# Kernel tuning notes

Measured on AMD Instinct MI355X. Metric: run time of the kernel, lower is better.

Reference implementation:

```python
import jax, jax.numpy as jnp
import numpy as np

V, E, H, K = 8000, 100, 64, 17  # vocab, embed, hidden, num_tags (fixed by source)
B, T = 256, 512


def setup_inputs() -> dict:
    key = jax.random.key(0)
    ks = jax.random.split(key, 16)
    g = lambda i, shape: (jax.random.normal(ks[i], shape, jnp.float32) * 0.1)
    data = jax.random.randint(ks[0], (B, T), 0, V).astype(jnp.int32)
    mask = jnp.ones((B, T), dtype=bool)
    return {
        "data": data,
        "mask": mask,
        "emb": g(1, (V, E)),
        # PyTorch LSTM layout: gates stacked [i, f, g, o] along dim 0
        "Wih_f": g(2, (4 * H, E)), "Whh_f": g(3, (4 * H, H)),
        "bih_f": g(4, (4 * H,)), "bhh_f": g(5, (4 * H,)),
        "Wih_b": g(6, (4 * H, E)), "Whh_b": g(7, (4 * H, H)),
        "bih_b": g(8, (4 * H,)), "bhh_b": g(9, (4 * H,)),
        "W_out": g(10, (K, 2 * H)), "b_out": g(11, (K,)),
        "trans": g(12, (K, K)),            # trans[i, j] = score of i -> j
        "start_trans": g(13, (K,)),
        "end_trans": g(14, (K,)),
    }


def _lstm_dir(x, Wih, Whh, bih, bhh, reverse):
    # x: [B, T, E] -> hidden states [B, T, H]
    Bx, Tx, _ = x.shape
    Hx = Whh.shape[1]
    xs = jnp.swapaxes(x, 0, 1)  # [T, B, E]

    def step(carry, xt):
        h, c = carry
        gates = xt @ Wih.T + h @ Whh.T + bih + bhh  # [B, 4H]
        i, f, g, o = jnp.split(gates, 4, axis=-1)
        c = jax.nn.sigmoid(f) * c + jax.nn.sigmoid(i) * jnp.tanh(g)
        h = jax.nn.sigmoid(o) * jnp.tanh(c)
        return (h, c), h

    init = (jnp.zeros((Bx, Hx), x.dtype), jnp.zeros((Bx, Hx), x.dtype))
    _, hs = jax.lax.scan(step, init, xs, reverse=reverse)
    return jnp.swapaxes(hs, 0, 1)  # [B, T, H]


def _emissions(data, emb, Wih_f, Whh_f, bih_f, bhh_f, Wih_b, Whh_b, bih_b, bhh_b, W_out, b_out):
    x = emb[data]                                         # [B, T, E]
    hf = _lstm_dir(x, Wih_f, Whh_f, bih_f, bhh_f, False)  # [B, T, H]
    hb = _lstm_dir(x, Wih_b, Whh_b, bih_b, bhh_b, True)   # [B, T, H]
    h = jnp.concatenate([hf, hb], axis=-1)                # [B, T, 2H]
    return h @ W_out.T + b_out                            # [B, T, K]


def _viterbi(emission, mask, trans, start_trans, end_trans):
    Bx, Tx, Kx = emission.shape
    score = start_trans[None, :] + emission[:, 0]         # [B, K]
    em = jnp.swapaxes(emission, 0, 1)[1:]                 # [T-1, B, K]
    mk = jnp.swapaxes(mask, 0, 1)[1:]                     # [T-1, B]
    ident = jnp.arange(Kx)

    def step(score, inp):
        emit_t, m_t = inp
        # cand[b, i, j] = score[b, i] + trans[i, j] + emit_t[b, j]
        cand = score[:, :, None] + trans[None] + emit_t[:, None, :]
        new = cand.max(axis=1)
        bp = cand.argmax(axis=1)
        score = jnp.where(m_t[:, None], new, score)
        bp = jnp.where(m_t[:, None], bp, ident[None, :])
        return score, bp

    score, bps = jax.lax.scan(step, score, (em, mk))       # bps: [T-1, B, K]
    final = score + end_trans[None, :]
    best_score = final.max(axis=1)                         # [B]
    last = final.argmax(axis=1)                            # [B]

    def back(tag, bp_t):
        prev = jnp.take_along_axis(bp_t, tag[:, None], axis=1)[:, 0]
        return prev, prev

    _, prevs = jax.lax.scan(back, last, bps, reverse=True)  # [T-1, B]
    paths = jnp.concatenate([prevs, last[None, :]], axis=0).T  # [B, T]
    return best_score, paths


def reference(data, mask, emb, Wih_f, Whh_f, bih_f, bhh_f, Wih_b, Whh_b, bih_b, bhh_b,
              W_out, b_out, trans, start_trans, end_trans):
    emission = _emissions(data, emb, Wih_f, Whh_f, bih_f, bhh_f,
                          Wih_b, Whh_b, bih_b, bhh_b, W_out, b_out)
    return _viterbi(emission, mask, trans, start_trans, end_trans)
```

## Files before the change

kernel.cpp:

```cpp
#include <hip/hip_runtime.h>
#include <hip/hip_bf16.h>

typedef unsigned int u32;
typedef unsigned char u8;

#define B_ 256
#define T_ 512
#define E_ 100
#define H_ 64
#define K_ 17
#define V_ 8000

#define WS_G     0
#define WS_H     16384000
#define WS_EMIT  83492864
#define WS_BP    92405760
#define WS_LAST  96600064

#define PINF4(v) asm volatile("" : "+v"((v).x), "+v"((v).y), "+v"((v).z), "+v"((v).w))

__device__ __forceinline__ float qp_xor1(float v) {
  int r = __builtin_amdgcn_update_dpp(0, __builtin_bit_cast(int, v), 0xB1, 0xF, 0xF, true);
  return __builtin_bit_cast(float, r);
}
__device__ __forceinline__ float qp_xor2(float v) {
  int r = __builtin_amdgcn_update_dpp(0, __builtin_bit_cast(int, v), 0x4E, 0xF, 0xF, true);
  return __builtin_bit_cast(float, r);
}

__global__ __launch_bounds__(256)
__attribute__((amdgpu_waves_per_eu(2, 2)))
void k1_build_G(
    const float* __restrict__ emb,
    const float* __restrict__ Wih_f,
    const float* __restrict__ bih_f,
    const float* __restrict__ bhh_f,
    const float* __restrict__ Wih_b,
    const float* __restrict__ bih_b,
    const float* __restrict__ bhh_b,
    float* __restrict__ G)
{
  __shared__ float xl[32 * E_];
  int v0 = blockIdx.x * 32;
  int dir = blockIdx.y;
  int tid = threadIdx.x;
  const float* Wih = dir ? Wih_b : Wih_f;
  const float* bih = dir ? bih_b : bih_f;
  const float* bhh = dir ? bhh_b : bhh_f;

  for (int i = tid; i < 32 * E_; i += 256) xl[i] = emb[v0 * E_ + i];

  int u = tid >> 2, g = tid & 3;
  int row = (g << 6) + u;
  const float* wr = Wih + row * E_;
#define LDA(name, q) float4 name = *reinterpret_cast<const float4*>(wr + 4 * (q)); PINF4(name)
  LDA(A0,0);  LDA(A1,1);  LDA(A2,2);  LDA(A3,3);  LDA(A4,4);
  LDA(A5,5);  LDA(A6,6);  LDA(A7,7);  LDA(A8,8);  LDA(A9,9);
  LDA(A10,10);LDA(A11,11);LDA(A12,12);LDA(A13,13);LDA(A14,14);
  LDA(A15,15);LDA(A16,16);LDA(A17,17);LDA(A18,18);LDA(A19,19);
  LDA(A20,20);LDA(A21,21);LDA(A22,22);LDA(A23,23);LDA(A24,24);
#undef LDA
  float bias = __fadd_rn(bih[row], bhh[row]);
  __syncthreads();

  float* Gd = G + (size_t)dir * V_ * 256;
  for (int vi = 0; vi < 32; ++vi) {
    const float* xp = &xl[vi * E_];
    float a0 = bias, a1 = 0.f, a2 = 0.f, a3 = 0.f;
#define K1F(Aq, q) { float4 x4 = *reinterpret_cast<const float4*>(xp + 4 * (q)); \
    a0 = fmaf(Aq.x, x4.x, a0); a1 = fmaf(Aq.y, x4.y, a1); \
    a2 = fmaf(Aq.z, x4.z, a2); a3 = fmaf(Aq.w, x4.w, a3); }
    K1F(A0,0)  K1F(A1,1)  K1F(A2,2)  K1F(A3,3)  K1F(A4,4)
    K1F(A5,5)  K1F(A6,6)  K1F(A7,7)  K1F(A8,8)  K1F(A9,9)
    K1F(A10,10)K1F(A11,11)K1F(A12,12)K1F(A13,13)K1F(A14,14)
    K1F(A15,15)K1F(A16,16)K1F(A17,17)K1F(A18,18)K1F(A19,19)
    K1F(A20,20)K1F(A21,21)K1F(A22,22)K1F(A23,23)K1F(A24,24)
#undef K1F
    Gd[(v0 + vi) * 256 + tid] = (a0 + a1) + (a2 + a3);
  }
}

__global__ __launch_bounds__(256)
__attribute__((amdgpu_waves_per_eu(2, 2)))
void k2_lstm(
    const int* __restrict__ data,
    const float* __restrict__ G,
    const float* __restrict__ Whh_f,
    const float* __restrict__ Whh_b,
    float* __restrict__ hout)
{
  __shared__ __align__(16) float hls[2][64];
  __shared__ int tok_lds[T_ + 8];
  int bid = blockIdx.x;
  int b = bid & 255;
  int dir = bid >> 8;
  int tid = threadIdx.x;
  int w = tid >> 6, l = tid & 63;
  int ul = l >> 2;
  int kq = l & 3;
  int u = (w << 4) + ul;
  const float* Whh = dir ? Whh_b : Whh_f;
  const float* wb = Whh + u * 64 + (kq << 4);

#define LDW(name, g, q) float4 name = *reinterpret_cast<const float4*>(wb + (g) * 4096 + 4 * (q)); PINF4(name)
  LDW(W00,0,0); LDW(W01,0,1); LDW(W02,0,2); LDW(W03,0,3);
  LDW(W10,1,0); LDW(W11,1,1); LDW(W12,1,2); LDW(W13,1,3);
  LDW(W20,2,0); LDW(W21,2,1); LDW(W22,2,2); LDW(W23,2,3);
  LDW(W30,3,0); LDW(W31,3,1); LDW(W32,3,2); LDW(W33,3,3);
#undef LDW

  const int* tokp = data + b * T_;
  for (int i = tid; i < T_; i += 256)
    tok_lds[i] = tokp[dir ? (T_ - 1 - i) : i];
  if (tid < 8) tok_lds[T_ + tid] = 0;
  if (tid < 64) hls[0][tid] = 0.0f;
  __syncthreads();

  float c = 0.0f;
  const float* Gd = G + (size_t)dir * V_ * 256;
  float* hob = hout + ((size_t)(dir * B_ + b)) * T_ * H_;
  float* hop = hob + (dir ? (T_ - 1) * H_ : 0) + u;
  int hstep = dir ? -H_ : H_;
  const float L2E = 1.4426950408889634f;

  float4 gq0, gq1, gq2, gq3;
  {
    int t0 = __builtin_amdgcn_readfirstlane(tok_lds[0]);
    int t1 = __builtin_amdgcn_readfirstlane(tok_lds[1]);
    int t2 = __builtin_amdgcn_readfirstlane(tok_lds[2]);
    int t3 = __builtin_amdgcn_readfirstlane(tok_lds[3]);
    gq0 = *reinterpret_cast<const float4*>(Gd + ((size_t)t0 << 8) + (u << 2));
    gq1 = *reinterpret_cast<const float4*>(Gd + ((size_t)t1 << 8) + (u << 2));
    gq2 = *reinterpret_cast<const float4*>(Gd + ((size_t)t2 << 8) + (u << 2));
    gq3 = *reinterpret_cast<const float4*>(Gd + ((size_t)t3 << 8) + (u << 2));
  }
  int tk_next = tok_lds[4];

  int cur = 0;
  for (int s = 0; s < T_; ++s) {
    int tokn = __builtin_amdgcn_readfirstlane(tk_next);
    float4 gq4 = *reinterpret_cast<const float4*>(Gd + ((size_t)tokn << 8) + (u << 2));
    tk_next = tok_lds[s + 5];

    const float* hq = hls[cur] + (kq << 4);
    float4 h0 = *reinterpret_cast<const float4*>(hq + 0);
    float4 h1 = *reinterpret_cast<const float4*>(hq + 4);
    float4 h2 = *reinterpret_cast<const float4*>(hq + 8);
    float4 h3 = *reinterpret_cast<const float4*>(hq + 12);
#define GDOT(res, Wa, Wb, Wc, Wd) float res; { \
    float b0 = Wa.x * h0.x; float b1 = Wa.y * h0.y; float b2 = Wa.z * h0.z; float b3 = Wa.w * h0.w; \
    b0 = fmaf(Wb.x, h1.x, b0); b1 = fmaf(Wb.y, h1.y, b1); b2 = fmaf(Wb.z, h1.z, b2); b3 = fmaf(Wb.w, h1.w, b3); \
    b0 = fmaf(Wc.x, h2.x, b0); b1 = fmaf(Wc.y, h2.y, b1); b2 = fmaf(Wc.z, h2.z, b2); b3 = fmaf(Wc.w, h2.w, b3); \
    b0 = fmaf(Wd.x, h3.x, b0); b1 = fmaf(Wd.y, h3.y, b1); b2 = fmaf(Wd.z, h3.z, b2); b3 = fmaf(Wd.w, h3.w, b3); \
    res = (b0 + b1) + (b2 + b3); }
    GDOT(acc0, W00, W01, W02, W03)
    GDOT(acc1, W10, W11, W12, W13)
    GDOT(acc2, W20, W21, W22, W23)
    GDOT(acc3, W30, W31, W32, W33)
#undef GDOT
    float t0 = acc0 + qp_xor1(acc0); float f0 = t0 + qp_xor2(t0);
    float t1 = acc1 + qp_xor1(acc1); float f1 = t1 + qp_xor2(t1);
    float t2 = acc2 + qp_xor1(acc2); float f2 = t2 + qp_xor2(t2);
    float t3 = acc3 + qp_xor1(acc3); float f3 = t3 + qp_xor2(t3);
    float xi = f0 + gq0.x;
    float xf = f1 + gq0.y;
    float xg = f2 + gq0.z;
    float xo = f3 + gq0.w;
    float si = __builtin_amdgcn_rcpf(1.0f + __builtin_amdgcn_exp2f(xi * (-L2E)));
    float sf = __builtin_amdgcn_rcpf(1.0f + __builtin_amdgcn_exp2f(xf * (-L2E)));
    float tg = fmaf(2.0f, __builtin_amdgcn_rcpf(1.0f + __builtin_amdgcn_exp2f(xg * (-2.0f * L2E))), -1.0f);
    float so = __builtin_amdgcn_rcpf(1.0f + __builtin_amdgcn_exp2f(xo * (-L2E)));
    c = __fadd_rn(__fmul_rn(sf, c), __fmul_rn(si, tg));
    float tc = fmaf(2.0f, __builtin_amdgcn_rcpf(1.0f + __builtin_amdgcn_exp2f(c * (-2.0f * L2E))), -1.0f);
    float hn = __fmul_rn(so, tc);
    if (kq == 0) {
      hls[cur ^ 1][u] = hn;
      *hop = hn;
    }
    hop += hstep;
    asm volatile("s_waitcnt lgkmcnt(0)\n\ts_barrier" ::: "memory");
    cur ^= 1;
    gq0 = gq1; gq1 = gq2; gq2 = gq3; gq3 = gq4;
  }
}

__global__ __launch_bounds__(256) void k3_emit(
    const float* __restrict__ hbuf,
    const float* __restrict__ W_out,
    const float* __restrict__ b_out,
    float* __restrict__ emit)
{
  __shared__ float hl[64][132];
  __shared__ float Wl[17][132];
  int tid = threadIdx.x;
  int p0 = blockIdx.x * 64;
  const float* hf = hbuf;
  const float* hb = hbuf + (size_t)B_ * T_ * H_;
#pragma unroll
  for (int i = 0; i < 4; ++i) {
    int idx = tid + i * 256;
    int pos = idx >> 4, e4 = idx & 15;
    float4 v = reinterpret_cast<const float4*>(hf + (size_t)p0 * 64)[idx];
    *reinterpret_cast<float4*>(&hl[pos][e4 * 4]) = v;
    float4 v2 = reinterpret_cast<const float4*>(hb + (size_t)p0 * 64)[idx];
    *reinterpret_cast<float4*>(&hl[pos][64 + e4 * 4]) = v2;
  }
  for (int i = tid; i < 17 * 128; i += 256) {
    int k = i >> 7, e = i & 127;
    Wl[k][e] = W_out[i];
  }
  __syncthreads();

  int pos = tid >> 2, ks = tid & 3;
  float acc[5] = {0.f, 0.f, 0.f, 0.f, 0.f};
#pragma unroll
  for (int e4 = 0; e4 < 32; ++e4) {
    float4 x4 = *reinterpret_cast<const float4*>(&hl[pos][e4 * 4]);
#pragma unroll
    for (int kk = 0; kk < 5; ++kk) {
      int k = ks + kk * 4;
      if (k < K_) {
        float4 w4 = *reinterpret_cast<const float4*>(&Wl[k][e4 * 4]);
        acc[kk] = fmaf(x4.x, w4.x, acc[kk]);
        acc[kk] = fmaf(x4.y, w4.y, acc[kk]);
        acc[kk] = fmaf(x4.z, w4.z, acc[kk]);
        acc[kk] = fmaf(x4.w, w4.w, acc[kk]);
      }
    }
  }
#pragma unroll
  for (int kk = 0; kk < 5; ++kk) {
    int k = ks + kk * 4;
    if (k < K_)
      emit[(size_t)(p0 + pos) * K_ + k] = __fadd_rn(acc[kk], b_out[k]);
  }
}

#define AMAX(vA, iA, vB, iB) { bool tk_ = (vB) > (vA); if (tk_) { vA = (vB); iA = (iB); } }

__global__ __launch_bounds__(64) void k4_viterbi(
    const float* __restrict__ emit,
    const float* __restrict__ trans,
    const float* __restrict__ start_trans,
    const float* __restrict__ end_trans,
    u8* __restrict__ bp,
    int* __restrict__ last,
    float* __restrict__ out)
{
  int b = blockIdx.x;
  int l = threadIdx.x;
  int ic = l >> 5;
  int hbase = l & 32;
  int j = l & 31;
  int jc = (j < K_) ? j : 0;
  int i0 = ic ? 9 : 0;
  int cnt = ic ? 8 : 9;
  float tr0 = trans[(i0 + 0) * K_ + jc];
  float tr1 = trans[(i0 + 1) * K_ + jc];
  float tr2 = trans[(i0 + 2) * K_ + jc];
  float tr3 = trans[(i0 + 3) * K_ + jc];
  float tr4 = trans[(i0 + 4) * K_ + jc];
  float tr5 = trans[(i0 + 5) * K_ + jc];
  float tr6 = trans[(i0 + 6) * K_ + jc];
  float tr7 = trans[(i0 + 7) * K_ + jc];
  float tr8 = (cnt > 8) ? trans[(i0 + 8) * K_ + jc] : -__builtin_inff();
  asm volatile("" : "+v"(tr0), "+v"(tr1), "+v"(tr2), "+v"(tr3), "+v"(tr4),
                    "+v"(tr5), "+v"(tr6), "+v"(tr7), "+v"(tr8));
  const float* eb = emit + (size_t)b * T_ * K_;
  float endt = end_trans[jc];
  float s = __fadd_rn(start_trans[jc], eb[jc]);
  u8* bpb = bp + (size_t)b * T_ * 32;
  float er0 = eb[1 * K_ + jc];
  float er1 = eb[2 * K_ + jc];
  float er2 = eb[3 * K_ + jc];
  float er3 = eb[4 * K_ + jc];

  for (int t = 1; t < T_; ++t) {
    float ej = er0;
    er0 = er1; er1 = er2; er2 = er3;
    if (t + 4 < T_) er3 = eb[(size_t)(t + 4) * K_ + jc];
    float p0 = __shfl(s, hbase + i0 + 0, 64);
    float p1 = __shfl(s, hbase + i0 + 1, 64);
    float p2 = __shfl(s, hbase + i0 + 2, 64);
    float p3 = __shfl(s, hbase + i0 + 3, 64);
    float p4 = __shfl(s, hbase + i0 + 4, 64);
    float p5 = __shfl(s, hbase + i0 + 5, 64);
    float p6 = __shfl(s, hbase + i0 + 6, 64);
    float p7 = __shfl(s, hbase + i0 + 7, 64);
    float p8 = __shfl(s, hbase + i0 + 8, 64);
    float c0 = __fadd_rn(__fadd_rn(p0, tr0), ej);
    float c1 = __fadd_rn(__fadd_rn(p1, tr1), ej);
    float c2 = __fadd_rn(__fadd_rn(p2, tr2), ej);
    float c3 = __fadd_rn(__fadd_rn(p3, tr3), ej);
    float c4 = __fadd_rn(__fadd_rn(p4, tr4), ej);
    float c5 = __fadd_rn(__fadd_rn(p5, tr5), ej);
    float c6 = __fadd_rn(__fadd_rn(p6, tr6), ej);
    float c7 = __fadd_rn(__fadd_rn(p7, tr7), ej);
    float c8 = __fadd_rn(__fadd_rn(p8, tr8), ej);
    float v01 = c0; int x01 = i0;     AMAX(v01, x01, c1, i0 + 1);
    float v23 = c2; int x23 = i0 + 2; AMAX(v23, x23, c3, i0 + 3);
    float v45 = c4; int x45 = i0 + 4; AMAX(v45, x45, c5, i0 + 5);
    float v67 = c6; int x67 = i0 + 6; AMAX(v67, x67, c7, i0 + 7);
    AMAX(v01, x01, v23, x23);
    AMAX(v45, x45, v67, x67);
    AMAX(v01, x01, v45, x45);
    AMAX(v01, x01, c8, i0 + 8);
    float m = v01; int idx = x01;
    float m2 = __shfl_xor(m, 32, 64);
    int idx2 = __shfl_xor(idx, 32, 64);
    bool take = (m2 > m) || ((m2 == m) && (idx2 < idx));
    if (take) { m = m2; idx = idx2; }
    s = m;
    if (ic == 0 && j < K_) bpb[(size_t)(t - 1) * 32 + j] = (u8)idx;
  }
  float fin = __fadd_rn(s, endt);
  float bm = __shfl(fin, hbase, 64);
  int bi = 0;
#pragma unroll
  for (int jj = 1; jj < K_; ++jj) {
    float v = __shfl(fin, hbase + jj, 64);
    if (v > bm) { bm = v; bi = jj; }
  }
  if (l == 0) {
    out[b] = bm;
    last[b] = bi;
    out[256 + (size_t)b * T_ + (T_ - 1)] = (float)bi;
  }
}

__global__ __launch_bounds__(64) void k5_backtrace(
    const u8* __restrict__ bp,
    const int* __restrict__ last,
    float* __restrict__ out)
{
  int b = blockIdx.x * 64 + threadIdx.x;
  const u8* base = bp + (size_t)b * T_ * 32;
  int tag = last[b];
  float* ob = out + 256 + (size_t)b * T_;
  uint4 A0[8], A1[8];
  u32 B0[8], B1[8];
#pragma unroll
  for (int q = 0; q < 8; ++q) {
    const u8* p = base + (size_t)(510 - q) * 32;
    A0[q] = *reinterpret_cast<const uint4*>(p);
    B0[q] = *reinterpret_cast<const u32*>(p + 16);
  }
  int t0 = 510;
  for (int pair = 0; pair < 32; ++pair) {
#pragma unroll
    for (int q = 0; q < 8; ++q) {
      int tn = t0 - 8 - q;
      if (tn >= 0) {
        const u8* p = base + (size_t)tn * 32;
        A1[q] = *reinterpret_cast<const uint4*>(p);
        B1[q] = *reinterpret_cast<const u32*>(p + 16);
      }
    }
#pragma unroll
    for (int q = 0; q < 8; ++q) {
      int t = t0 - q;
      if (t >= 0) {
        uint4 Av = A0[q]; u32 Bw = B0[q];
        u32 dw = (tag < 8) ? ((tag < 4) ? Av.x : Av.y) : ((tag < 12) ? Av.z : Av.w);
        dw = (tag < 16) ? dw : Bw;
        tag = (int)((dw >> ((tag & 3) * 8)) & 0xffu);
        ob[t] = (float)tag;
      }
    }
#pragma unroll
    for (int q = 0; q < 8; ++q) {
      int tn = t0 - 16 - q;
      if (tn >= 0) {
        const u8* p = base + (size_t)tn * 32;
        A0[q] = *reinterpret_cast<const uint4*>(p);
        B0[q] = *reinterpret_cast<const u32*>(p + 16);
      }
    }
#pragma unroll
    for (int q = 0; q < 8; ++q) {
      int t = t0 - 8 - q;
      if (t >= 0) {
        uint4 Av = A1[q]; u32 Bw = B1[q];
        u32 dw = (tag < 8) ? ((tag < 4) ? Av.x : Av.y) : ((tag < 12) ? Av.z : Av.w);
        dw = (tag < 16) ? dw : Bw;
        tag = (int)((dw >> ((tag & 3) * 8)) & 0xffu);
        ob[t] = (float)tag;
      }
    }
    t0 -= 16;
  }
}

extern "C" void kernel_launch(void* const* d_in, const int* in_sizes, int n_in,
                              void* d_out, int out_size, void* d_ws, size_t ws_size,
                              hipStream_t stream) {
  const int*   data  = (const int*)d_in[0];
  const float* emb   = (const float*)d_in[2];
  const float* Wih_f = (const float*)d_in[3];
  const float* Whh_f = (const float*)d_in[4];
  const float* bih_f = (const float*)d_in[5];
  const float* bhh_f = (const float*)d_in[6];
  const float* Wih_b = (const float*)d_in[7];
  const float* Whh_b = (const float*)d_in[8];
  const float* bih_b = (const float*)d_in[9];
  const float* bhh_b = (const float*)d_in[10];
  const float* W_out = (const float*)d_in[11];
  const float* b_out = (const float*)d_in[12];
  const float* trans = (const float*)d_in[13];
  const float* start_trans = (const float*)d_in[14];
  const float* end_trans   = (const float*)d_in[15];

  char* ws = (char*)d_ws;
  float* G    = (float*)(ws + WS_G);
  float* hbuf = (float*)(ws + WS_H);
  float* emit = (float*)(ws + WS_EMIT);
  u8*    bp   = (u8*)(ws + WS_BP);
  int*   lastp = (int*)(ws + WS_LAST);
  float* out = (float*)d_out;

  k1_build_G<<<dim3(250, 2), 256, 0, stream>>>(emb, Wih_f, bih_f, bhh_f,
                                               Wih_b, bih_b, bhh_b, G);
  k2_lstm<<<512, 256, 0, stream>>>(data, G, Whh_f, Whh_b, hbuf);
  k3_emit<<<2048, 256, 0, stream>>>(hbuf, W_out, b_out, emit);
  k4_viterbi<<<256, 64, 0, stream>>>(emit, trans, start_trans, end_trans,
                                     bp, lastp, out);
  k5_backtrace<<<4, 64, 0, stream>>>(bp, lastp, out);
}
```

Before: 668.2 us.

## Use packed FMA in LSTM, register-resident emit projection, readlane-based Viterbi

```diff
diff --git a/kernel.cpp b/kernel.cpp
--- a/kernel.cpp
+++ b/kernel.cpp
@@ -3,6 +3,7 @@
 
 typedef unsigned int u32;
 typedef unsigned char u8;
+typedef __attribute__((ext_vector_type(2))) float f2;
 
 #define B_ 256
 #define T_ 512
@@ -18,6 +19,8 @@
 #define WS_LAST  96600064
 
 #define PINF4(v) asm volatile("" : "+v"((v).x), "+v"((v).y), "+v"((v).z), "+v"((v).w))
+#define PINF2(v) asm volatile("" : "+v"(v))
+#define FMA2(a, b, c) __builtin_elementwise_fma((a), (b), (c))
 
 __device__ __forceinline__ float qp_xor1(float v) {
   int r = __builtin_amdgcn_update_dpp(0, __builtin_bit_cast(int, v), 0xB1, 0xF, 0xF, true);
@@ -26,6 +29,9 @@
 __device__ __forceinline__ float qp_xor2(float v) {
   int r = __builtin_amdgcn_update_dpp(0, __builtin_bit_cast(int, v), 0x4E, 0xF, 0xF, true);
   return __builtin_bit_cast(float, r);
+}
+__device__ __forceinline__ float rdl(float v, int lane) {
+  return __builtin_bit_cast(float, __builtin_amdgcn_readlane(__builtin_bit_cast(int, v), lane));
 }
 
 __global__ __launch_bounds__(256)
@@ -100,13 +106,16 @@
   int kq = l & 3;
   int u = (w << 4) + ul;
   const float* Whh = dir ? Whh_b : Whh_f;
-  const float* wb = Whh + u * 64 + (kq << 4);
-
-#define LDW(name, g, q) float4 name = *reinterpret_cast<const float4*>(wb + (g) * 4096 + 4 * (q)); PINF4(name)
-  LDW(W00,0,0); LDW(W01,0,1); LDW(W02,0,2); LDW(W03,0,3);
-  LDW(W10,1,0); LDW(W11,1,1); LDW(W12,1,2); LDW(W13,1,3);
-  LDW(W20,2,0); LDW(W21,2,1); LDW(W22,2,2); LDW(W23,2,3);
-  LDW(W30,3,0); LDW(W31,3,1); LDW(W32,3,2); LDW(W33,3,3);
+  const f2* wb2 = reinterpret_cast<const f2*>(Whh + u * 64 + (kq << 4));
+
+#define LDW(pre, g) \
+  f2 pre##0 = wb2[(g)*2048+0]; f2 pre##1 = wb2[(g)*2048+1]; \
+  f2 pre##2 = wb2[(g)*2048+2]; f2 pre##3 = wb2[(g)*2048+3]; \
+  f2 pre##4 = wb2[(g)*2048+4]; f2 pre##5 = wb2[(g)*2048+5]; \
+  f2 pre##6 = wb2[(g)*2048+6]; f2 pre##7 = wb2[(g)*2048+7]; \
+  PINF2(pre##0); PINF2(pre##1); PINF2(pre##2); PINF2(pre##3); \
+  PINF2(pre##4); PINF2(pre##5); PINF2(pre##6); PINF2(pre##7)
+  LDW(Wa, 0); LDW(Wb, 1); LDW(Wc, 2); LDW(Wd, 3);
 #undef LDW
 
   const int* tokp = data + b * T_;
@@ -137,34 +146,31 @@
   int tk_next = tok_lds[4];
 
   int cur = 0;
+#pragma unroll 2
   for (int s = 0; s < T_; ++s) {
     int tokn = __builtin_amdgcn_readfirstlane(tk_next);
     float4 gq4 = *reinterpret_cast<const float4*>(Gd + ((size_t)tokn << 8) + (u << 2));
     tk_next = tok_lds[s + 5];
 
-    const float* hq = hls[cur] + (kq << 4);
-    float4 h0 = *reinterpret_cast<const float4*>(hq + 0);
-    float4 h1 = *reinterpret_cast<const float4*>(hq + 4);
-    float4 h2 = *reinterpret_cast<const float4*>(hq + 8);
-    float4 h3 = *reinterpret_cast<const float4*>(hq + 12);
-#define GDOT(res, Wa, Wb, Wc, Wd) float res; { \
-    float b0 = Wa.x * h0.x; float b1 = Wa.y * h0.y; float b2 = Wa.z * h0.z; float b3 = Wa.w * h0.w; \
-    b0 = fmaf(Wb.x, h1.x, b0); b1 = fmaf(Wb.y, h1.y, b1); b2 = fmaf(Wb.z, h1.z, b2); b3 = fmaf(Wb.w, h1.w, b3); \
-    b0 = fmaf(Wc.x, h2.x, b0); b1 = fmaf(Wc.y, h2.y, b1); b2 = fmaf(Wc.z, h2.z, b2); b3 = fmaf(Wc.w, h2.w, b3); \
-    b0 = fmaf(Wd.x, h3.x, b0); b1 = fmaf(Wd.y, h3.y, b1); b2 = fmaf(Wd.z, h3.z, b2); b3 = fmaf(Wd.w, h3.w, b3); \
-    res = (b0 + b1) + (b2 + b3); }
-    GDOT(acc0, W00, W01, W02, W03)
-    GDOT(acc1, W10, W11, W12, W13)
-    GDOT(acc2, W20, W21, W22, W23)
-    GDOT(acc3, W30, W31, W32, W33)
+    const f2* hq2 = reinterpret_cast<const f2*>(hls[cur] + (kq << 4));
+    f2 ha = hq2[0], hb2 = hq2[1], hc = hq2[2], hd = hq2[3];
+    f2 he = hq2[4], hf2 = hq2[5], hg = hq2[6], hh = hq2[7];
+#define GDOT(res, W0,W1,W2,W3,W4,W5,W6,W7) float res; { \
+    f2 c01 = W0 * ha;  c01 = FMA2(W2, hc, c01); c01 = FMA2(W4, he, c01); c01 = FMA2(W6, hg, c01); \
+    f2 c23 = W1 * hb2; c23 = FMA2(W3, hd, c23); c23 = FMA2(W5, hf2, c23); c23 = FMA2(W7, hh, c23); \
+    res = (c01.x + c01.y) + (c23.x + c23.y); }
+    GDOT(acc0, Wa0,Wa1,Wa2,Wa3,Wa4,Wa5,Wa6,Wa7)
+    GDOT(acc1, Wb0,Wb1,Wb2,Wb3,Wb4,Wb5,Wb6,Wb7)
+    GDOT(acc2, Wc0,Wc1,Wc2,Wc3,Wc4,Wc5,Wc6,Wc7)
+    GDOT(acc3, Wd0,Wd1,Wd2,Wd3,Wd4,Wd5,Wd6,Wd7)
 #undef GDOT
     float t0 = acc0 + qp_xor1(acc0); float f0 = t0 + qp_xor2(t0);
     float t1 = acc1 + qp_xor1(acc1); float f1 = t1 + qp_xor2(t1);
-    float t2 = acc2 + qp_xor1(acc2); float f2 = t2 + qp_xor2(t2);
+    float t2 = acc2 + qp_xor1(acc2); float f2v = t2 + qp_xor2(t2);
     float t3 = acc3 + qp_xor1(acc3); float f3 = t3 + qp_xor2(t3);
     float xi = f0 + gq0.x;
     float xf = f1 + gq0.y;
-    float xg = f2 + gq0.z;
+    float xg = f2v + gq0.z;
     float xo = f3 + gq0.w;
     float si = __builtin_amdgcn_rcpf(1.0f + __builtin_amdgcn_exp2f(xi * (-L2E)));
     float sf = __builtin_amdgcn_rcpf(1.0f + __builtin_amdgcn_exp2f(xf * (-L2E)));
@@ -184,55 +190,45 @@
   }
 }
 
-__global__ __launch_bounds__(256) void k3_emit(
+__global__ __launch_bounds__(256)
+__attribute__((amdgpu_waves_per_eu(2, 2)))
+void k3_emit(
     const float* __restrict__ hbuf,
     const float* __restrict__ W_out,
     const float* __restrict__ b_out,
     float* __restrict__ emit)
 {
-  __shared__ float hl[64][132];
-  __shared__ float Wl[17][132];
-  int tid = threadIdx.x;
-  int p0 = blockIdx.x * 64;
-  const float* hf = hbuf;
-  const float* hb = hbuf + (size_t)B_ * T_ * H_;
-#pragma unroll
-  for (int i = 0; i < 4; ++i) {
-    int idx = tid + i * 256;
-    int pos = idx >> 4, e4 = idx & 15;
-    float4 v = reinterpret_cast<const float4*>(hf + (size_t)p0 * 64)[idx];
-    *reinterpret_cast<float4*>(&hl[pos][e4 * 4]) = v;
-    float4 v2 = reinterpret_cast<const float4*>(hb + (size_t)p0 * 64)[idx];
-    *reinterpret_cast<float4*>(&hl[pos][64 + e4 * 4]) = v2;
-  }
-  for (int i = tid; i < 17 * 128; i += 256) {
-    int k = i >> 7, e = i & 127;
-    Wl[k][e] = W_out[i];
-  }
-  __syncthreads();
-
-  int pos = tid >> 2, ks = tid & 3;
-  float acc[5] = {0.f, 0.f, 0.f, 0.f, 0.f};
-#pragma unroll
-  for (int e4 = 0; e4 < 32; ++e4) {
-    float4 x4 = *reinterpret_cast<const float4*>(&hl[pos][e4 * 4]);
-#pragma unroll
-    for (int kk = 0; kk < 5; ++kk) {
-      int k = ks + kk * 4;
-      if (k < K_) {
-        float4 w4 = *reinterpret_cast<const float4*>(&Wl[k][e4 * 4]);
-        acc[kk] = fmaf(x4.x, w4.x, acc[kk]);
-        acc[kk] = fmaf(x4.y, w4.y, acc[kk]);
-        acc[kk] = fmaf(x4.z, w4.z, acc[kk]);
-        acc[kk] = fmaf(x4.w, w4.w, acc[kk]);
-      }
-    }
-  }
-#pragma unroll
-  for (int kk = 0; kk < 5; ++kk) {
-    int k = ks + kk * 4;
-    if (k < K_)
-      emit[(size_t)(p0 + pos) * K_ + k] = __fadd_rn(acc[kk], b_out[k]);
+  int pos = blockIdx.x * 256 + threadIdx.x;
+  const float* hfp = hbuf + (size_t)pos * 64;
+  const float* hbp = hbuf + (size_t)B_ * T_ * 64 + (size_t)pos * 64;
+#define LDH(name, base, q) float4 name = *reinterpret_cast<const float4*>((base) + 4 * (q)); PINF4(name)
+  LDH(H0, hfp,0);  LDH(H1, hfp,1);  LDH(H2, hfp,2);  LDH(H3, hfp,3);
+  LDH(H4, hfp,4);  LDH(H5, hfp,5);  LDH(H6, hfp,6);  LDH(H7, hfp,7);
+  LDH(H8, hfp,8);  LDH(H9, hfp,9);  LDH(H10,hfp,10); LDH(H11,hfp,11);
+  LDH(H12,hfp,12); LDH(H13,hfp,13); LDH(H14,hfp,14); LDH(H15,hfp,15);
+  LDH(H16,hbp,0);  LDH(H17,hbp,1);  LDH(H18,hbp,2);  LDH(H19,hbp,3);
+  LDH(H20,hbp,4);  LDH(H21,hbp,5);  LDH(H22,hbp,6);  LDH(H23,hbp,7);
+  LDH(H24,hbp,8);  LDH(H25,hbp,9);  LDH(H26,hbp,10); LDH(H27,hbp,11);
+  LDH(H28,hbp,12); LDH(H29,hbp,13); LDH(H30,hbp,14); LDH(H31,hbp,15);
+#undef LDH
+  float* ep = emit + (size_t)pos * K_;
+#pragma unroll 1
+  for (int k = 0; k < K_; ++k) {
+    const float* wk = W_out + k * 128;
+    float a0 = 0.f, a1 = 0.f, a2 = 0.f, a3 = 0.f;
+#define K3F(Hq, q) { \
+    a0 = fmaf(Hq.x, wk[4*(q)+0], a0); a1 = fmaf(Hq.y, wk[4*(q)+1], a1); \
+    a2 = fmaf(Hq.z, wk[4*(q)+2], a2); a3 = fmaf(Hq.w, wk[4*(q)+3], a3); }
+    K3F(H0,0)  K3F(H1,1)  K3F(H2,2)  K3F(H3,3)
+    K3F(H4,4)  K3F(H5,5)  K3F(H6,6)  K3F(H7,7)
+    K3F(H8,8)  K3F(H9,9)  K3F(H10,10)K3F(H11,11)
+    K3F(H12,12)K3F(H13,13)K3F(H14,14)K3F(H15,15)
+    K3F(H16,16)K3F(H17,17)K3F(H18,18)K3F(H19,19)
+    K3F(H20,20)K3F(H21,21)K3F(H22,22)K3F(H23,23)
+    K3F(H24,24)K3F(H25,25)K3F(H26,26)K3F(H27,27)
+    K3F(H28,28)K3F(H29,29)K3F(H30,30)K3F(H31,31)
+#undef K3F
+    ep[k] = __fadd_rn((a0 + a1) + (a2 + a3), b_out[k]);
   }
 }
 
@@ -249,82 +245,95 @@
 {
   int b = blockIdx.x;
   int l = threadIdx.x;
-  int ic = l >> 5;
-  int hbase = l & 32;
-  int j = l & 31;
-  int jc = (j < K_) ? j : 0;
-  int i0 = ic ? 9 : 0;
-  int cnt = ic ? 8 : 9;
-  float tr0 = trans[(i0 + 0) * K_ + jc];
-  float tr1 = trans[(i0 + 1) * K_ + jc];
-  float tr2 = trans[(i0 + 2) * K_ + jc];
-  float tr3 = trans[(i0 + 3) * K_ + jc];
-  float tr4 = trans[(i0 + 4) * K_ + jc];
-  float tr5 = trans[(i0 + 5) * K_ + jc];
-  float tr6 = trans[(i0 + 6) * K_ + jc];
-  float tr7 = trans[(i0 + 7) * K_ + jc];
-  float tr8 = (cnt > 8) ? trans[(i0 + 8) * K_ + jc] : -__builtin_inff();
-  asm volatile("" : "+v"(tr0), "+v"(tr1), "+v"(tr2), "+v"(tr3), "+v"(tr4),
-                    "+v"(tr5), "+v"(tr6), "+v"(tr7), "+v"(tr8));
+  int jc = (l < K_) ? l : 0;
+  float tr0  = trans[ 0 * K_ + jc], tr1  = trans[ 1 * K_ + jc];
+  float tr2  = trans[ 2 * K_ + jc], tr3  = trans[ 3 * K_ + jc];
+  float tr4  = trans[ 4 * K_ + jc], tr5  = trans[ 5 * K_ + jc];
+  float tr6  = trans[ 6 * K_ + jc], tr7  = trans[ 7 * K_ + jc];
+  float tr8  = trans[ 8 * K_ + jc], tr9  = trans[ 9 * K_ + jc];
+  float tr10 = trans[10 * K_ + jc], tr11 = trans[11 * K_ + jc];
+  float tr12 = trans[12 * K_ + jc], tr13 = trans[13 * K_ + jc];
+  float tr14 = trans[14 * K_ + jc], tr15 = trans[15 * K_ + jc];
+  float tr16 = trans[16 * K_ + jc];
   const float* eb = emit + (size_t)b * T_ * K_;
   float endt = end_trans[jc];
   float s = __fadd_rn(start_trans[jc], eb[jc]);
   u8* bpb = bp + (size_t)b * T_ * 32;
-  float er0 = eb[1 * K_ + jc];
-  float er1 = eb[2 * K_ + jc];
-  float er2 = eb[3 * K_ + jc];
-  float er3 = eb[4 * K_ + jc];
-
+  float er0 = eb[1 * K_ + jc], er1 = eb[2 * K_ + jc];
+  float er2 = eb[3 * K_ + jc], er3 = eb[4 * K_ + jc];
+  float er4 = eb[5 * K_ + jc], er5 = eb[6 * K_ + jc];
+  float er6 = eb[7 * K_ + jc], er7 = eb[8 * K_ + jc];
+
+#pragma unroll 4
   for (int t = 1; t < T_; ++t) {
     float ej = er0;
-    er0 = er1; er1 = er2; er2 = er3;
-    if (t + 4 < T_) er3 = eb[(size_t)(t + 4) * K_ + jc];
-    float p0 = __shfl(s, hbase + i0 + 0, 64);
-    float p1 = __shfl(s, hbase + i0 + 1, 64);
-    float p2 = __shfl(s, hbase + i0 + 2, 64);
-    float p3 = __shfl(s, hbase + i0 + 3, 64);
-    float p4 = __shfl(s, hbase + i0 + 4, 64);
-    float p5 = __shfl(s, hbase + i0 + 5, 64);
-    float p6 = __shfl(s, hbase + i0 + 6, 64);
-    float p7 = __shfl(s, hbase + i0 + 7, 64);
-    float p8 = __shfl(s, hbase + i0 + 8, 64);
-    float c0 = __fadd_rn(__fadd_rn(p0, tr0), ej);
-    float c1 = __fadd_rn(__fadd_rn(p1, tr1), ej);
-    float c2 = __fadd_rn(__fadd_rn(p2, tr2), ej);
-    float c3 = __fadd_rn(__fadd_rn(p3, tr3), ej);
-    float c4 = __fadd_rn(__fadd_rn(p4, tr4), ej);
-    float c5 = __fadd_rn(__fadd_rn(p5, tr5), ej);
-    float c6 = __fadd_rn(__fadd_rn(p6, tr6), ej);
-    float c7 = __fadd_rn(__fadd_rn(p7, tr7), ej);
-    float c8 = __fadd_rn(__fadd_rn(p8, tr8), ej);
-    float v01 = c0; int x01 = i0;     AMAX(v01, x01, c1, i0 + 1);
-    float v23 = c2; int x23 = i0 + 2; AMAX(v23, x23, c3, i0 + 3);
-    float v45 = c4; int x45 = i0 + 4; AMAX(v45, x45, c5, i0 + 5);
-    float v67 = c6; int x67 = i0 + 6; AMAX(v67, x67, c7, i0 + 7);
-    AMAX(v01, x01, v23, x23);
-    AMAX(v45, x45, v67, x67);
-    AMAX(v01, x01, v45, x45);
-    AMAX(v01, x01, c8, i0 + 8);
-    float m = v01; int idx = x01;
-    float m2 = __shfl_xor(m, 32, 64);
-    int idx2 = __shfl_xor(idx, 32, 64);
-    bool take = (m2 > m) || ((m2 == m) && (idx2 < idx));
-    if (take) { m = m2; idx = idx2; }
-    s = m;
-    if (ic == 0 && j < K_) bpb[(size_t)(t - 1) * 32 + j] = (u8)idx;
+    er0 = er1; er1 = er2; er2 = er3; er3 = er4;
+    er4 = er5; er5 = er6; er6 = er7;
+    int tn = (t + 8 < T_) ? (t + 8) : (T_ - 1);
+    er7 = eb[(size_t)tn * K_ + jc];
+    float sg0  = rdl(s, 0),  sg1  = rdl(s, 1),  sg2  = rdl(s, 2);
+    float sg3  = rdl(s, 3),  sg4  = rdl(s, 4),  sg5  = rdl(s, 5);
+    float sg6  = rdl(s, 6),  sg7  = rdl(s, 7),  sg8  = rdl(s, 8);
+    float sg9  = rdl(s, 9),  sg10 = rdl(s, 10), sg11 = rdl(s, 11);
+    float sg12 = rdl(s, 12), sg13 = rdl(s, 13), sg14 = rdl(s, 14);
+    float sg15 = rdl(s, 15), sg16 = rdl(s, 16);
+    float c0  = __fadd_rn(__fadd_rn(sg0,  tr0),  ej);
+    float c1  = __fadd_rn(__fadd_rn(sg1,  tr1),  ej);
+    float c2  = __fadd_rn(__fadd_rn(sg2,  tr2),  ej);
+    float c3  = __fadd_rn(__fadd_rn(sg3,  tr3),  ej);
+    float c4  = __fadd_rn(__fadd_rn(sg4,  tr4),  ej);
+    float c5  = __fadd_rn(__fadd_rn(sg5,  tr5),  ej);
+    float c6  = __fadd_rn(__fadd_rn(sg6,  tr6),  ej);
+    float c7  = __fadd_rn(__fadd_rn(sg7,  tr7),  ej);
+    float c8  = __fadd_rn(__fadd_rn(sg8,  tr8),  ej);
+    float c9  = __fadd_rn(__fadd_rn(sg9,  tr9),  ej);
+    float c10 = __fadd_rn(__fadd_rn(sg10, tr10), ej);
+    float c11 = __fadd_rn(__fadd_rn(sg11, tr11), ej);
+    float c12 = __fadd_rn(__fadd_rn(sg12, tr12), ej);
+    float c13 = __fadd_rn(__fadd_rn(sg13, tr13), ej);
+    float c14 = __fadd_rn(__fadd_rn(sg14, tr14), ej);
+    float c15 = __fadd_rn(__fadd_rn(sg15, tr15), ej);
+    float c16 = __fadd_rn(__fadd_rn(sg16, tr16), ej);
+    float v0 = c0;  int x0 = 0;  AMAX(v0, x0, c1, 1);
+    float v1 = c2;  int x1 = 2;  AMAX(v1, x1, c3, 3);
+    float v2 = c4;  int x2 = 4;  AMAX(v2, x2, c5, 5);
+    float v3 = c6;  int x3 = 6;  AMAX(v3, x3, c7, 7);
+    float v4 = c8;  int x4 = 8;  AMAX(v4, x4, c9, 9);
+    float v5 = c10; int x5 = 10; AMAX(v5, x5, c11, 11);
+    float v6 = c12; int x6 = 12; AMAX(v6, x6, c13, 13);
+    float v7 = c14; int x7 = 14; AMAX(v7, x7, c15, 15);
+    AMAX(v0, x0, v1, x1); AMAX(v2, x2, v3, x3);
+    AMAX(v4, x4, v5, x5); AMAX(v6, x6, v7, x7);
+    AMAX(v0, x0, v2, x2); AMAX(v4, x4, v6, x6);
+    AMAX(v0, x0, v4, x4);
+    AMAX(v0, x0, c16, 16);
+    s = v0;
+    if (l < K_) bpb[(size_t)(t - 1) * 32 + l] = (u8)x0;
   }
   float fin = __fadd_rn(s, endt);
-  float bm = __shfl(fin, hbase, 64);
-  int bi = 0;
-#pragma unroll
-  for (int jj = 1; jj < K_; ++jj) {
-    float v = __shfl(fin, hbase + jj, 64);
-    if (v > bm) { bm = v; bi = jj; }
-  }
+  float g0  = rdl(fin, 0),  g1  = rdl(fin, 1),  g2  = rdl(fin, 2);
+  float g3  = rdl(fin, 3),  g4  = rdl(fin, 4),  g5  = rdl(fin, 5);
+  float g6  = rdl(fin, 6),  g7  = rdl(fin, 7),  g8  = rdl(fin, 8);
+  float g9  = rdl(fin, 9),  g10 = rdl(fin, 10), g11 = rdl(fin, 11);
+  float g12 = rdl(fin, 12), g13 = rdl(fin, 13), g14 = rdl(fin, 14);
+  float g15 = rdl(fin, 15), g16 = rdl(fin, 16);
+  float w0 = g0;  int y0 = 0;  AMAX(w0, y0, g1, 1);
+  float w1 = g2;  int y1 = 2;  AMAX(w1, y1, g3, 3);
+  float w2 = g4;  int y2 = 4;  AMAX(w2, y2, g5, 5);
+  float w3 = g6;  int y3 = 6;  AMAX(w3, y3, g7, 7);
+  float w4 = g8;  int y4 = 8;  AMAX(w4, y4, g9, 9);
+  float w5 = g10; int y5 = 10; AMAX(w5, y5, g11, 11);
+  float w6 = g12; int y6 = 12; AMAX(w6, y6, g13, 13);
+  float w7 = g14; int y7 = 14; AMAX(w7, y7, g15, 15);
+  AMAX(w0, y0, w1, y1); AMAX(w2, y2, w3, y3);
+  AMAX(w4, y4, w5, y5); AMAX(w6, y6, w7, y7);
+  AMAX(w0, y0, w2, y2); AMAX(w4, y4, w6, y6);
+  AMAX(w0, y0, w4, y4);
+  AMAX(w0, y0, g16, 16);
   if (l == 0) {
-    out[b] = bm;
-    last[b] = bi;
-    out[256 + (size_t)b * T_ + (T_ - 1)] = (float)bi;
+    out[b] = w0;
+    last[b] = y0;
+    out[256 + (size_t)b * T_ + (T_ - 1)] = (float)y0;
   }
 }
 
@@ -421,7 +430,7 @@
   k1_build_G<<<dim3(250, 2), 256, 0, stream>>>(emb, Wih_f, bih_f, bhh_f,
                                                Wih_b, bih_b, bhh_b, G);
   k2_lstm<<<512, 256, 0, stream>>>(data, G, Whh_f, Whh_b, hbuf);
-  k3_emit<<<2048, 256, 0, stream>>>(hbuf, W_out, b_out, emit);
+  k3_emit<<<512, 256, 0, stream>>>(hbuf, W_out, b_out, emit);
   k4_viterbi<<<256, 64, 0, stream>>>(emit, trans, start_trans, end_trans,
                                      bp, lastp, out);
   k5_backtrace<<<4, 64, 0, stream>>>(bp, lastp, out);
```

Result: slower. 744.8 us (+11.5%).
